# Kernel tuning notes

Measured on AMD Instinct MI355X. Metric: run time of the kernel, lower is better.

The kernel has to match this reference:

```python
import jax, jax.numpy as jnp
import numpy as np

B, T, CV, DIM = 1, 1024, 8, 2048
NH, HD, W = 32, 64, 8
BMM = NH * HD


def swa_transform(x, window):
    # x: (b, t, cv, d) -> (b, t, window*cv, d)
    # matches torch pad-front + unfold + transpose + reshape: window-major, char-minor
    b, t, cv, d = x.shape
    xp = jnp.pad(x, ((0, 0), (window - 1, 0), (0, 0), (0, 0)))
    wins = jnp.stack([xp[:, w:w + t] for w in range(window)], axis=2)  # (b,t,W,cv,d)
    return wins.reshape(b, t, window * cv, d)


def rope(x, freqs):
    # interleaved-pair RoPE (rotary_embedding_torch default, theta=10000)
    # x: (..., hd); freqs broadcastable against x[..., 0::2]
    cos, sin = jnp.cos(freqs), jnp.sin(freqs)
    x1, x2 = x[..., 0::2], x[..., 1::2]
    return jnp.stack([x1 * cos - x2 * sin, x1 * sin + x2 * cos], axis=-1).reshape(x.shape)


def setup_inputs() -> dict:
    key = jax.random.key(0)
    ks = jax.random.split(key, 6)
    s = 0.02
    return {
        "x": jax.random.normal(ks[0], (B, T, DIM), dtype=jnp.float32),
        "chars": jax.random.normal(ks[1], (B, T, CV, DIM), dtype=jnp.float32),
        "wq": jax.random.normal(ks[2], (BMM, DIM), dtype=jnp.float32) * s,
        "wk": jax.random.normal(ks[3], (BMM, DIM), dtype=jnp.float32) * s,
        "wv": jax.random.normal(ks[4], (BMM, DIM), dtype=jnp.float32) * s,
        "wo": jax.random.normal(ks[5], (DIM, BMM), dtype=jnp.float32) * s,
    }


def reference(x, chars, wq, wk, wv, wo):
    b, t = x.shape[0], x.shape[1]
    cv = chars.shape[2]
    wc = W * cv

    q = x @ wq.T                     # (b, t, BMM)
    k = chars @ wk.T                 # (b, t, cv, BMM)
    v = chars @ wv.T

    k = swa_transform(k, W)          # (b, t, W*cv, BMM)
    v = swa_transform(v, W)

    q = q.reshape(b, t, NH, HD).transpose(0, 2, 1, 3)          # (b, nh, t, hd)
    k = k.reshape(b, t, wc, NH, HD).transpose(0, 3, 1, 2, 4)   # (b, nh, t, wc, hd)
    v = v.reshape(b, t, wc, NH, HD).transpose(0, 3, 1, 2, 4)   # (b, nh, t, wc, hd)

    inv_freq = 1.0 / (10000.0 ** (jnp.arange(0, HD, 2, dtype=jnp.float32) / HD))
    freqs = jnp.arange(t, dtype=jnp.float32)[:, None] * inv_freq  # (t, hd/2)

    q = rope(q, freqs)                       # rotate over token axis (-2)
    k = rope(k, freqs[:, None, :])           # rotate over token axis (-3), broadcast over window

    scores = jnp.einsum('bhtd,bhtkd->bhtk', q, k) / np.float32(np.sqrt(HD))
    attn = jax.nn.softmax(scores, axis=-1)   # (b, nh, t, wc)
    out = jnp.einsum('bhtk,bhtkd->bhtd', attn, v)
    out = out.transpose(0, 2, 1, 3).reshape(b, t, NH * HD)
    return out @ wo.T
```

## Files before the change

### kernel.cpp

```cpp
#include <hip/hip_runtime.h>
#include <hip/hip_bf16.h>
#include <cstdint>
#include <cstddef>

static constexpr int kT   = 1024;
static constexpr int kCV  = 8;
static constexpr int kDim = 2048;
static constexpr int kNH  = 32;
static constexpr int kHD  = 64;
static constexpr int kW   = 8;
static constexpr int kK   = 2048;

using bf16_t = __hip_bfloat16;

typedef __attribute__((ext_vector_type(8))) __bf16 bf16x8;
typedef __attribute__((ext_vector_type(4))) float  f32x4;

__device__ __forceinline__ float bf_bits_to_f32(unsigned short u) {
    union { unsigned int i; float f; } c;
    c.i = ((unsigned int)u) << 16;
    return c.f;
}

struct CastArgs {
    const float* src[6];
    bf16_t*      dst[6];
    int          cum[7];
};

__global__ void cast_all(CastArgs a, int total_chunks) {
    const int c = blockIdx.x * blockDim.x + threadIdx.x;
    if (c >= total_chunks) return;
    int r = 0;
#pragma unroll
    for (int i = 1; i <= 5; ++i) r += (c >= a.cum[i]) ? 1 : 0;
    const int local = c - a.cum[r];
    const float* s = a.src[r] + (size_t)local * 8;
    bf16_t*      d = a.dst[r] + (size_t)local * 8;
    const float4 lo = *reinterpret_cast<const float4*>(s);
    const float4 hi = *reinterpret_cast<const float4*>(s + 4);
    union { bf16_t h[8]; uint4 u; } o;
    o.h[0] = __float2bfloat16(lo.x); o.h[1] = __float2bfloat16(lo.y);
    o.h[2] = __float2bfloat16(lo.z); o.h[3] = __float2bfloat16(lo.w);
    o.h[4] = __float2bfloat16(hi.x); o.h[5] = __float2bfloat16(hi.y);
    o.h[6] = __float2bfloat16(hi.z); o.h[7] = __float2bfloat16(hi.w);
    *reinterpret_cast<uint4*>(d) = o.u;
}

__device__ __forceinline__ void gemm256_body(const bf16_t* __restrict__ A,
                                             const bf16_t* __restrict__ Wt,
                                             bf16_t* __restrict__ C,
                                             int bm, int bn, int ldc,
                                             bf16_t* smem) {
    const int tid  = threadIdx.x;
    const int wave = tid >> 6;
    const int lane = tid & 63;
    const int l16  = lane & 15;
    const int quad = lane >> 4;
    const int wm   = (wave >> 2) * 128;
    const int wn   = (wave & 3) * 64;

    f32x4 acc[8][4];
#pragma unroll
    for (int i = 0; i < 8; ++i)
#pragma unroll
        for (int j = 0; j < 4; ++j) acc[i][j] = (f32x4)0.0f;

    const int srow = tid >> 3;
    const int jg   = (tid & 7) ^ (srow & 7);
    const bf16_t* gA = A  + (size_t)(bm + srow) * kK + jg * 8;
    const bf16_t* gB = Wt + (size_t)(bn + srow) * kK + jg * 8;
    const int ldsw = wave * 512;

    auto stage = [&](int kt, int p) {
        const int k0 = kt * 64;
        bf16_t* As = smem + p * 32768;
        bf16_t* Bs = As + 16384;
#pragma unroll
        for (int i = 0; i < 4; ++i)
            __builtin_amdgcn_global_load_lds(
                (const __attribute__((address_space(1))) void*)(gA + (size_t)i * 64 * kK + k0),
                (__attribute__((address_space(3))) void*)(As + i * 4096 + ldsw),
                16, 0, 0);
#pragma unroll
        for (int i = 0; i < 4; ++i)
            __builtin_amdgcn_global_load_lds(
                (const __attribute__((address_space(1))) void*)(gB + (size_t)i * 64 * kK + k0),
                (__attribute__((address_space(3))) void*)(Bs + i * 4096 + ldsw),
                16, 0, 0);
    };

    bf16x8 af[8], bq[4];
    auto rdfrags = [&](int p, int ph) {
        const bf16_t* As = smem + p * 32768;
        const bf16_t* Bs = As + 16384;
        const int jla = (ph * 4 + quad) ^ (l16 & 7);
#pragma unroll
        for (int i = 0; i < 8; ++i)
            af[i] = *reinterpret_cast<const bf16x8*>(
                &As[(wm + i * 16 + l16) * 64 + jla * 8]);
#pragma unroll
        for (int j = 0; j < 4; ++j)
            bq[j] = *reinterpret_cast<const bf16x8*>(
                &Bs[(wn + j * 16 + l16) * 64 + jla * 8]);
    };
    auto domfma = [&]() {
#pragma unroll
        for (int i = 0; i < 8; ++i)
#pragma unroll
            for (int j = 0; j < 4; ++j)
                acc[i][j] = __builtin_amdgcn_mfma_f32_16x16x32_bf16(
                    af[i], bq[j], acc[i][j], 0, 0, 0);
    };

    stage(0, 0);
    stage(1, 1);
    asm volatile("s_waitcnt vmcnt(8)" ::: "memory");
    __builtin_amdgcn_s_barrier();

    static_assert(kK / 64 == 32, "NT");
    int p = 0;
    for (int t = 0; t < 30; ++t) {
        rdfrags(p, 0);
        domfma();
        rdfrags(p, 1);
        asm volatile("s_waitcnt lgkmcnt(0)" ::: "memory");
        __builtin_amdgcn_s_barrier();
        stage(t + 2, p);
        __builtin_amdgcn_s_setprio(1);
        domfma();
        __builtin_amdgcn_s_setprio(0);
        asm volatile("s_waitcnt vmcnt(8)" ::: "memory");
        __builtin_amdgcn_s_barrier();
        p ^= 1;
    }
    rdfrags(p, 0); domfma();
    rdfrags(p, 1);
    __builtin_amdgcn_s_setprio(1);
    domfma();
    __builtin_amdgcn_s_setprio(0);
    asm volatile("s_waitcnt vmcnt(0)" ::: "memory");
    __builtin_amdgcn_s_barrier();
    p ^= 1;
    rdfrags(p, 0); domfma();
    rdfrags(p, 1); domfma();

#pragma unroll
    for (int i = 0; i < 8; ++i) {
#pragma unroll
        for (int rr = 0; rr < 4; ++rr) {
            const int row = bm + wm + i * 16 + quad * 4 + rr;
#pragma unroll
            for (int j = 0; j < 4; ++j) {
                const int col = bn + wn + j * 16 + l16;
                C[(size_t)row * ldc + col] = __float2bfloat16(acc[i][j][rr]);
            }
        }
    }
}

__global__ __launch_bounds__(512, 2) void proj256_kernel(
    const bf16_t* __restrict__ xb, const bf16_t* __restrict__ cb,
    const bf16_t* __restrict__ wqb, const bf16_t* __restrict__ wkvb,
    bf16_t* __restrict__ qb, bf16_t* __restrict__ kvb) {
    extern __shared__ bf16_t smem[];
    const int bid = blockIdx.x;
    if (bid < 512) {
        const int bm = (bid >> 4) * 256;
        const int bn = (bid & 15) * 256;
        gemm256_body(cb, wkvb, kvb, bm, bn, 4096, smem);
    } else {
        const int t  = bid - 512;
        const int bm = (t >> 3) * 256;
        const int bn = (t & 7) * 256;
        gemm256_body(xb, wqb, qb, bm, bn, 2048, smem);
    }
}

template <bool ATOMIC>
__device__ __forceinline__ void gemm_body128(const bf16_t* __restrict__ A,
                                             const bf16_t* __restrict__ Wt,
                                             float* __restrict__ C,
                                             int bm, int bn, int ldc,
                                             int kbeg, int kend) {
    __shared__ bf16_t As[128 * 64];
    __shared__ bf16_t Bs[128 * 64];

    const int tid  = threadIdx.x;
    const int wave = tid >> 6;
    const int lane = tid & 63;
    const int l16  = lane & 15;
    const int quad = lane >> 4;
    const int wm   = (wave >> 1) * 64;
    const int wn   = (wave & 1) * 64;

    f32x4 acc[4][4];
#pragma unroll
    for (int i = 0; i < 4; ++i)
#pragma unroll
        for (int j = 0; j < 4; ++j) acc[i][j] = (f32x4)0.0f;

    const int srow = tid >> 3;
    const int jgs  = (tid & 7) ^ (srow & 7);
    const bf16_t* gA = A  + (size_t)(bm + srow) * kK + jgs * 8;
    const bf16_t* gB = Wt + (size_t)(bn + srow) * kK + jgs * 8;

    for (int k0 = kbeg; k0 < kend; k0 += 64) {
#pragma unroll
        for (int i = 0; i < 4; ++i) {
            __builtin_amdgcn_global_load_lds(
                (const __attribute__((address_space(1))) void*)(gA + (size_t)i * 32 * kK + k0),
                (__attribute__((address_space(3))) void*)(As + i * 2048 + wave * 512),
                16, 0, 0);
            __builtin_amdgcn_global_load_lds(
                (const __attribute__((address_space(1))) void*)(gB + (size_t)i * 32 * kK + k0),
                (__attribute__((address_space(3))) void*)(Bs + i * 2048 + wave * 512),
                16, 0, 0);
        }
        __syncthreads();

#pragma unroll
        for (int ph = 0; ph < 2; ++ph) {
            bf16x8 af[4], bfr[4];
#pragma unroll
            for (int i = 0; i < 4; ++i) {
                const int jla = (ph * 4 + quad) ^ (l16 & 7);
                af[i]  = *reinterpret_cast<const bf16x8*>(
                    &As[(wm + i * 16 + l16) * 64 + jla * 8]);
                bfr[i] = *reinterpret_cast<const bf16x8*>(
                    &Bs[(wn + i * 16 + l16) * 64 + jla * 8]);
            }
#pragma unroll
            for (int i = 0; i < 4; ++i)
#pragma unroll
                for (int j = 0; j < 4; ++j)
                    acc[i][j] = __builtin_amdgcn_mfma_f32_16x16x32_bf16(
                        af[i], bfr[j], acc[i][j], 0, 0, 0);
        }
        __syncthreads();
    }

#pragma unroll
    for (int i = 0; i < 4; ++i) {
#pragma unroll
        for (int rr = 0; rr < 4; ++rr) {
            const int row = bm + wm + i * 16 + quad * 4 + rr;
#pragma unroll
            for (int j = 0; j < 4; ++j) {
                const int col = bn + wn + j * 16 + l16;
                if constexpr (ATOMIC) {
                    atomicAdd(&C[(size_t)row * ldc + col], acc[i][j][rr]);
                } else {
                    C[(size_t)row * ldc + col] = acc[i][j][rr];
                }
            }
        }
    }
}

__global__ __launch_bounds__(256, 3) void out_gemm(
    const bf16_t* __restrict__ ob, const bf16_t* __restrict__ wob,
    float* __restrict__ out) {
    const int tile = blockIdx.x & 127;
    const int ks   = blockIdx.x >> 7;
    const int bm = (tile >> 4) * 128;
    const int bn = (tile & 15) * 128;
    gemm_body128<true>(ob, wob, out, bm, bn, 2048, ks * 1024, ks * 1024 + 1024);
}

static constexpr int kTT   = 16;
static constexpr int kSRC  = kTT + kW - 1;
static constexpr int kROWS = kSRC * kCV;
static constexpr int kLDK  = 72;

__global__ __launch_bounds__(1024) void attn_kernel(
    const bf16_t* __restrict__ qb,
    const bf16_t* __restrict__ kvb,
    bf16_t* __restrict__ ob) {
    __shared__ unsigned short kl[kROWS * kLDK];
    __shared__ unsigned short vl[kROWS * kLDK];
    __shared__ float ql[kTT * 64];
    __shared__ float al[kTT * 64];

    const int t0   = blockIdx.x * kTT;
    const int h    = blockIdx.y;
    const int tid  = threadIdx.x;
    const int wave = tid >> 6;
    const int lane = tid & 63;

    ql[tid] = __bfloat162float(qb[(size_t)(t0 + wave) * kDim + h * kHD + lane]);

    const long long grow0 = (long long)(t0 - (kW - 1)) * kCV;
#pragma unroll
    for (int c = tid; c < kROWS * 8; c += 1024) {
        const int r   = c >> 3;
        const int sub = c & 7;
        const long long grow = grow0 + r;
        uint4 kd = make_uint4(0, 0, 0, 0), vd = make_uint4(0, 0, 0, 0);
        if (grow >= 0) {
            const size_t gb = (size_t)grow * 4096 + h * kHD + sub * 8;
            kd = *reinterpret_cast<const uint4*>(kvb + gb);
            vd = *reinterpret_cast<const uint4*>(kvb + gb + 2048);
        }
        *reinterpret_cast<uint4*>(&kl[r * kLDK + sub * 8]) = kd;
        *reinterpret_cast<uint4*>(&vl[r * kLDK + sub * 8]) = vd;
    }
    __syncthreads();

    const int r = wave * kCV + lane;
    float s = 0.0f;
#pragma unroll
    for (int c = 0; c < 8; ++c) {
        union { uint4 u; unsigned short us[8]; } kv;
        kv.u = *reinterpret_cast<const uint4*>(&kl[r * kLDK + c * 8]);
        const float4 qa = *reinterpret_cast<const float4*>(&ql[wave * 64 + c * 8]);
        const float4 qc = *reinterpret_cast<const float4*>(&ql[wave * 64 + c * 8 + 4]);
        s += bf_bits_to_f32(kv.us[0]) * qa.x + bf_bits_to_f32(kv.us[1]) * qa.y +
             bf_bits_to_f32(kv.us[2]) * qa.z + bf_bits_to_f32(kv.us[3]) * qa.w +
             bf_bits_to_f32(kv.us[4]) * qc.x + bf_bits_to_f32(kv.us[5]) * qc.y +
             bf_bits_to_f32(kv.us[6]) * qc.z + bf_bits_to_f32(kv.us[7]) * qc.w;
    }
    s *= 0.125f;

    float m = s;
#pragma unroll
    for (int off = 32; off; off >>= 1) m = fmaxf(m, __shfl_xor(m, off));
    const float e = __expf(s - m);
    float sum = e;
#pragma unroll
    for (int off = 32; off; off >>= 1) sum += __shfl_xor(sum, off);
    al[wave * 64 + lane] = e / sum;

    float o = 0.0f;
#pragma unroll
    for (int k2 = 0; k2 < 64; ++k2)
        o += al[wave * 64 + k2] * bf_bits_to_f32(vl[(wave * kCV + k2) * kLDK + lane]);
    ob[(size_t)(t0 + wave) * kDim + h * kHD + lane] = __float2bfloat16(o);
}

extern "C" void kernel_launch(void* const* d_in, const int* in_sizes, int n_in,
                              void* d_out, int out_size, void* d_ws,
                              size_t ws_size, hipStream_t stream) {
    const float* x     = (const float*)d_in[0];
    const float* chars = (const float*)d_in[1];
    const float* wq    = (const float*)d_in[2];
    const float* wk    = (const float*)d_in[3];
    const float* wv    = (const float*)d_in[4];
    const float* wo    = (const float*)d_in[5];
    float* out = (float*)d_out;

    char* p = (char*)d_ws;
    bf16_t* xb   = (bf16_t*)p; p += (size_t)kT * kDim * 2;
    bf16_t* cb   = (bf16_t*)p; p += (size_t)kT * kCV * kDim * 2;
    bf16_t* wqb  = (bf16_t*)p; p += (size_t)kDim * kDim * 2;
    bf16_t* wkvb = (bf16_t*)p; p += (size_t)2 * kDim * kDim * 2;
    bf16_t* wob  = (bf16_t*)p; p += (size_t)kDim * kDim * 2;
    bf16_t* qb   = (bf16_t*)p; p += (size_t)kT * kDim * 2;
    bf16_t* kvb  = (bf16_t*)p; p += (size_t)kT * kCV * 2 * kDim * 2;
    bf16_t* ob   = (bf16_t*)p; p += (size_t)kT * kDim * 2;

    static int attr_done = 0;
    if (!attr_done) {
        hipFuncSetAttribute(reinterpret_cast<const void*>(proj256_kernel),
                            hipFuncAttributeMaxDynamicSharedMemorySize, 131072);
        attr_done = 1;
    }

    hipMemsetAsync(out, 0, (size_t)kT * kDim * sizeof(float), stream);

    CastArgs ca;
    ca.src[0] = x;     ca.dst[0] = xb;
    ca.src[1] = chars; ca.dst[1] = cb;
    ca.src[2] = wq;    ca.dst[2] = wqb;
    ca.src[3] = wk;    ca.dst[3] = wkvb;
    ca.src[4] = wv;    ca.dst[4] = wkvb + (size_t)kDim * kDim;
    ca.src[5] = wo;    ca.dst[5] = wob;
    const int sizes[6] = {kT * kDim, kT * kCV * kDim, kDim * kDim,
                          kDim * kDim, kDim * kDim, kDim * kDim};
    int cum = 0;
    ca.cum[0] = 0;
    for (int i = 0; i < 6; ++i) { cum += sizes[i] / 8; ca.cum[i + 1] = cum; }
    cast_all<<<dim3((cum + 255) / 256), dim3(256), 0, stream>>>(ca, cum);

    proj256_kernel<<<dim3(544), dim3(512), 131072, stream>>>(
        xb, cb, wqb, wkvb, qb, kvb);

    attn_kernel<<<dim3(kT / kTT, kNH), dim3(1024), 0, stream>>>(qb, kvb, ob);

    out_gemm<<<dim3(256), dim3(256), 0, stream>>>(ob, wob, out);
}
```

Baseline: 386.8 us.

## Rework projection GEMM into 8-phase pipeline and split Q GEMM into 128 tiles

The 256x256 KV projection GEMM now runs an 8-phase schedule. Each phase loads a 32-row slice of A fragments and issues one half-tile global-to-LDS stage, so memory traffic is spread across the MFMA work instead of arriving in bursts. The Q projection switches from 32 blocks of 256x256 to 128 blocks of 128x128 using a simpler single-buffered kernel, which raises the block count for the tail. The change adds many more barriers per k-step, and the simpler Q path drops double buffering. The unused non-atomic template path in the output GEMM is removed.

```diff
diff --git a/kernel.cpp b/kernel.cpp
--- a/kernel.cpp
+++ b/kernel.cpp
@@ -47,18 +47,21 @@
     *reinterpret_cast<uint4*>(d) = o.u;
 }
 
-__device__ __forceinline__ void gemm256_body(const bf16_t* __restrict__ A,
-                                             const bf16_t* __restrict__ Wt,
-                                             bf16_t* __restrict__ C,
-                                             int bm, int bn, int ldc,
-                                             bf16_t* smem) {
+__device__ __forceinline__ void gemm256_8ph(const bf16_t* __restrict__ A,
+                                            const bf16_t* __restrict__ Wt,
+                                            bf16_t* __restrict__ C,
+                                            int bm, int bn, int ldc,
+                                            bf16_t* smem) {
     const int tid  = threadIdx.x;
     const int wave = tid >> 6;
     const int lane = tid & 63;
     const int l16  = lane & 15;
     const int quad = lane >> 4;
-    const int wm   = (wave >> 2) * 128;
-    const int wn   = (wave & 3) * 64;
+    const int wmi  = wave >> 2;
+    const int wni  = wave & 3;
+
+    const int slot0 = quad ^ (l16 & 7);
+    const int slot1 = slot0 ^ 4;
 
     f32x4 acc[8][4];
 #pragma unroll
@@ -67,99 +70,201 @@
         for (int j = 0; j < 4; ++j) acc[i][j] = (f32x4)0.0f;
 
     const int srow = tid >> 3;
-    const int jg   = (tid & 7) ^ (srow & 7);
-    const bf16_t* gA = A  + (size_t)(bm + srow) * kK + jg * 8;
-    const bf16_t* gB = Wt + (size_t)(bn + srow) * kK + jg * 8;
+    const int jg8  = (((tid & 7) ^ (srow & 7))) * 8;
+    const bf16_t* gAlo = A  + (size_t)(bm + srow) * kK + jg8;
+    const bf16_t* gAhi = gAlo + (size_t)128 * kK;
+    const bf16_t* gBlo = Wt + (size_t)(bn + srow) * kK + jg8;
+    const bf16_t* gBhi = gBlo + (size_t)128 * kK;
     const int ldsw = wave * 512;
 
-    auto stage = [&](int kt, int p) {
-        const int k0 = kt * 64;
-        bf16_t* As = smem + p * 32768;
-        bf16_t* Bs = As + 16384;
-#pragma unroll
-        for (int i = 0; i < 4; ++i)
+    auto stageA = [&](int tau, int hs) {
+        bf16_t* dst = smem + (tau & 1) * 32768 + hs * 8192 + ldsw;
+        const bf16_t* src = (hs ? gAhi : gAlo) + tau * 64;
+        __builtin_amdgcn_global_load_lds(
+            (const __attribute__((address_space(1))) void*)src,
+            (__attribute__((address_space(3))) void*)dst, 16, 0, 0);
+        __builtin_amdgcn_global_load_lds(
+            (const __attribute__((address_space(1))) void*)(src + (size_t)64 * kK),
+            (__attribute__((address_space(3))) void*)(dst + 4096), 16, 0, 0);
+    };
+    auto stageB = [&](int tau, int hs) {
+        bf16_t* dst = smem + (tau & 1) * 32768 + 16384 + hs * 8192 + ldsw;
+        const bf16_t* src = (hs ? gBhi : gBlo) + tau * 64;
+        __builtin_amdgcn_global_load_lds(
+            (const __attribute__((address_space(1))) void*)src,
+            (__attribute__((address_space(3))) void*)dst, 16, 0, 0);
+        __builtin_amdgcn_global_load_lds(
+            (const __attribute__((address_space(1))) void*)(src + (size_t)64 * kK),
+            (__attribute__((address_space(3))) void*)(dst + 4096), 16, 0, 0);
+    };
+
+    bf16x8 bq0[4], bq1[4];
+
+#define PH(P, Q, STG, VMW)                                                     \
+    {                                                                          \
+        const bf16_t* Ab = smem + (P) * 32768;                                 \
+        const bf16_t* Bb = Ab + 16384;                                         \
+        bf16x8 a0[2], a1[2];                                                   \
+        _Pragma("unroll")                                                      \
+        for (int ii = 0; ii < 2; ++ii) {                                       \
+            const int rb = (wmi * 128 + ((Q) * 2 + ii) * 16 + l16) * 64;       \
+            a0[ii] = *reinterpret_cast<const bf16x8*>(&Ab[rb + slot0 * 8]);    \
+            a1[ii] = *reinterpret_cast<const bf16x8*>(&Ab[rb + slot1 * 8]);    \
+        }                                                                      \
+        if ((Q) == 0) {                                                        \
+            _Pragma("unroll")                                                  \
+            for (int j = 0; j < 4; ++j) {                                      \
+                const int rb = (wni * 64 + j * 16 + l16) * 64;                 \
+                bq0[j] = *reinterpret_cast<const bf16x8*>(&Bb[rb + slot0 * 8]);\
+                bq1[j] = *reinterpret_cast<const bf16x8*>(&Bb[rb + slot1 * 8]);\
+            }                                                                  \
+        }                                                                      \
+        STG;                                                                   \
+        __builtin_amdgcn_s_barrier();                                          \
+        asm volatile("s_waitcnt lgkmcnt(0)" ::: "memory");                     \
+        __builtin_amdgcn_s_setprio(1);                                         \
+        _Pragma("unroll")                                                      \
+        for (int ii = 0; ii < 2; ++ii)                                         \
+            _Pragma("unroll")                                                  \
+            for (int j = 0; j < 4; ++j)                                        \
+                acc[(Q) * 2 + ii][j] = __builtin_amdgcn_mfma_f32_16x16x32_bf16(\
+                    a0[ii], bq0[j], acc[(Q) * 2 + ii][j], 0, 0, 0);            \
+        _Pragma("unroll")                                                      \
+        for (int ii = 0; ii < 2; ++ii)                                         \
+            _Pragma("unroll")                                                  \
+            for (int j = 0; j < 4; ++j)                                        \
+                acc[(Q) * 2 + ii][j] = __builtin_amdgcn_mfma_f32_16x16x32_bf16(\
+                    a1[ii], bq1[j], acc[(Q) * 2 + ii][j], 0, 0, 0);            \
+        __builtin_amdgcn_s_setprio(0);                                         \
+        VMW;                                                                   \
+        __builtin_amdgcn_s_barrier();                                          \
+    }
+
+#define VM4 asm volatile("s_waitcnt vmcnt(4)" ::: "memory")
+#define VM0 asm volatile("s_waitcnt vmcnt(0)" ::: "memory")
+
+    stageB(0, 1); stageB(0, 0); stageA(0, 1); stageA(0, 0);
+    stageB(1, 1); stageB(1, 0);
+    VM4;
+    __builtin_amdgcn_s_barrier();
+
+    for (int tt = 0; tt < 15; ++tt) {
+        const int t = tt * 2;
+        PH(0, 0, stageA(t + 1, 1), (void)0)
+        PH(0, 1, stageA(t + 1, 0), (void)0)
+        PH(0, 2, stageB(t + 2, 1), (void)0)
+        PH(0, 3, stageB(t + 2, 0), VM4)
+        PH(1, 0, stageA(t + 2, 1), (void)0)
+        PH(1, 1, stageA(t + 2, 0), (void)0)
+        PH(1, 2, stageB(t + 3, 1), (void)0)
+        PH(1, 3, stageB(t + 3, 0), VM4)
+    }
+    PH(0, 0, stageA(31, 1), (void)0)
+    PH(0, 1, stageA(31, 0), (void)0)
+    PH(0, 2, (void)0, (void)0)
+    PH(0, 3, (void)0, VM0)
+    PH(1, 0, (void)0, (void)0)
+    PH(1, 1, (void)0, (void)0)
+    PH(1, 2, (void)0, (void)0)
+    PH(1, 3, (void)0, (void)0)
+
+#undef PH
+#undef VM4
+#undef VM0
+
+#pragma unroll
+    for (int i = 0; i < 8; ++i) {
+#pragma unroll
+        for (int rr = 0; rr < 4; ++rr) {
+            const int row = bm + wmi * 128 + i * 16 + quad * 4 + rr;
+#pragma unroll
+            for (int j = 0; j < 4; ++j) {
+                const int col = bn + wni * 64 + j * 16 + l16;
+                C[(size_t)row * ldc + col] = __float2bfloat16(acc[i][j][rr]);
+            }
+        }
+    }
+}
+
+__device__ __forceinline__ void gemm128_8w(const bf16_t* __restrict__ A,
+                                           const bf16_t* __restrict__ Wt,
+                                           bf16_t* __restrict__ C,
+                                           int bm, int bn, int ldc,
+                                           bf16_t* smem) {
+    const int tid  = threadIdx.x;
+    const int wave = tid >> 6;
+    const int lane = tid & 63;
+    const int l16  = lane & 15;
+    const int quad = lane >> 4;
+    const int wmi  = wave >> 2;
+    const int wni  = wave & 3;
+
+    bf16_t* As = smem;
+    bf16_t* Bs = smem + 8192;
+
+    f32x4 acc[4][2];
+#pragma unroll
+    for (int i = 0; i < 4; ++i)
+#pragma unroll
+        for (int j = 0; j < 2; ++j) acc[i][j] = (f32x4)0.0f;
+
+    const int srow = tid >> 3;
+    const int jg8  = (((tid & 7) ^ (srow & 7))) * 8;
+    const bf16_t* gA = A  + (size_t)(bm + srow) * kK + jg8;
+    const bf16_t* gB = Wt + (size_t)(bn + srow) * kK + jg8;
+    const int ldsw = wave * 512;
+
+    for (int k0 = 0; k0 < kK; k0 += 64) {
+#pragma unroll
+        for (int i = 0; i < 2; ++i) {
             __builtin_amdgcn_global_load_lds(
                 (const __attribute__((address_space(1))) void*)(gA + (size_t)i * 64 * kK + k0),
                 (__attribute__((address_space(3))) void*)(As + i * 4096 + ldsw),
                 16, 0, 0);
-#pragma unroll
-        for (int i = 0; i < 4; ++i)
             __builtin_amdgcn_global_load_lds(
                 (const __attribute__((address_space(1))) void*)(gB + (size_t)i * 64 * kK + k0),
                 (__attribute__((address_space(3))) void*)(Bs + i * 4096 + ldsw),
                 16, 0, 0);
-    };
-
-    bf16x8 af[8], bq[4];
-    auto rdfrags = [&](int p, int ph) {
-        const bf16_t* As = smem + p * 32768;
-        const bf16_t* Bs = As + 16384;
-        const int jla = (ph * 4 + quad) ^ (l16 & 7);
-#pragma unroll
-        for (int i = 0; i < 8; ++i)
-            af[i] = *reinterpret_cast<const bf16x8*>(
-                &As[(wm + i * 16 + l16) * 64 + jla * 8]);
-#pragma unroll
-        for (int j = 0; j < 4; ++j)
-            bq[j] = *reinterpret_cast<const bf16x8*>(
-                &Bs[(wn + j * 16 + l16) * 64 + jla * 8]);
-    };
-    auto domfma = [&]() {
-#pragma unroll
-        for (int i = 0; i < 8; ++i)
-#pragma unroll
-            for (int j = 0; j < 4; ++j)
-                acc[i][j] = __builtin_amdgcn_mfma_f32_16x16x32_bf16(
-                    af[i], bq[j], acc[i][j], 0, 0, 0);
-    };
-
-    stage(0, 0);
-    stage(1, 1);
-    asm volatile("s_waitcnt vmcnt(8)" ::: "memory");
-    __builtin_amdgcn_s_barrier();
-
-    static_assert(kK / 64 == 32, "NT");
-    int p = 0;
-    for (int t = 0; t < 30; ++t) {
-        rdfrags(p, 0);
-        domfma();
-        rdfrags(p, 1);
-        asm volatile("s_waitcnt lgkmcnt(0)" ::: "memory");
-        __builtin_amdgcn_s_barrier();
-        stage(t + 2, p);
-        __builtin_amdgcn_s_setprio(1);
-        domfma();
-        __builtin_amdgcn_s_setprio(0);
-        asm volatile("s_waitcnt vmcnt(8)" ::: "memory");
-        __builtin_amdgcn_s_barrier();
-        p ^= 1;
-    }
-    rdfrags(p, 0); domfma();
-    rdfrags(p, 1);
-    __builtin_amdgcn_s_setprio(1);
-    domfma();
-    __builtin_amdgcn_s_setprio(0);
-    asm volatile("s_waitcnt vmcnt(0)" ::: "memory");
-    __builtin_amdgcn_s_barrier();
-    p ^= 1;
-    rdfrags(p, 0); domfma();
-    rdfrags(p, 1); domfma();
-
-#pragma unroll
-    for (int i = 0; i < 8; ++i) {
+        }
+        __syncthreads();
+
+#pragma unroll
+        for (int ph = 0; ph < 2; ++ph) {
+            const int jla = (ph * 4 + quad) ^ (l16 & 7);
+            bf16x8 af[4], bfr[2];
+#pragma unroll
+            for (int i = 0; i < 4; ++i)
+                af[i] = *reinterpret_cast<const bf16x8*>(
+                    &As[(wmi * 64 + i * 16 + l16) * 64 + jla * 8]);
+#pragma unroll
+            for (int j = 0; j < 2; ++j)
+                bfr[j] = *reinterpret_cast<const bf16x8*>(
+                    &Bs[(wni * 32 + j * 16 + l16) * 64 + jla * 8]);
+#pragma unroll
+            for (int i = 0; i < 4; ++i)
+#pragma unroll
+                for (int j = 0; j < 2; ++j)
+                    acc[i][j] = __builtin_amdgcn_mfma_f32_16x16x32_bf16(
+                        af[i], bfr[j], acc[i][j], 0, 0, 0);
+        }
+        __syncthreads();
+    }
+
+#pragma unroll
+    for (int i = 0; i < 4; ++i) {
 #pragma unroll
         for (int rr = 0; rr < 4; ++rr) {
-            const int row = bm + wm + i * 16 + quad * 4 + rr;
-#pragma unroll
-            for (int j = 0; j < 4; ++j) {
-                const int col = bn + wn + j * 16 + l16;
+            const int row = bm + wmi * 64 + i * 16 + quad * 4 + rr;
+#pragma unroll
+            for (int j = 0; j < 2; ++j) {
+                const int col = bn + wni * 32 + j * 16 + l16;
                 C[(size_t)row * ldc + col] = __float2bfloat16(acc[i][j][rr]);
             }
         }
     }
 }
 
-__global__ __launch_bounds__(512, 2) void proj256_kernel(
+__global__ __launch_bounds__(512, 2) void proj8_kernel(
     const bf16_t* __restrict__ xb, const bf16_t* __restrict__ cb,
     const bf16_t* __restrict__ wqb, const bf16_t* __restrict__ wkvb,
     bf16_t* __restrict__ qb, bf16_t* __restrict__ kvb) {
@@ -168,16 +273,15 @@
     if (bid < 512) {
         const int bm = (bid >> 4) * 256;
         const int bn = (bid & 15) * 256;
-        gemm256_body(cb, wkvb, kvb, bm, bn, 4096, smem);
+        gemm256_8ph(cb, wkvb, kvb, bm, bn, 4096, smem);
     } else {
         const int t  = bid - 512;
-        const int bm = (t >> 3) * 256;
-        const int bn = (t & 7) * 256;
-        gemm256_body(xb, wqb, qb, bm, bn, 2048, smem);
-    }
-}
-
-template <bool ATOMIC>
+        const int bm = (t >> 4) * 128;
+        const int bn = (t & 15) * 128;
+        gemm128_8w(xb, wqb, qb, bm, bn, 2048, smem);
+    }
+}
+
 __device__ __forceinline__ void gemm_body128(const bf16_t* __restrict__ A,
                                              const bf16_t* __restrict__ Wt,
                                              float* __restrict__ C,
@@ -248,11 +352,7 @@
 #pragma unroll
             for (int j = 0; j < 4; ++j) {
                 const int col = bn + wn + j * 16 + l16;
-                if constexpr (ATOMIC) {
-                    atomicAdd(&C[(size_t)row * ldc + col], acc[i][j][rr]);
-                } else {
-                    C[(size_t)row * ldc + col] = acc[i][j][rr];
-                }
+                atomicAdd(&C[(size_t)row * ldc + col], acc[i][j][rr]);
             }
         }
     }
@@ -265,7 +365,7 @@
     const int ks   = blockIdx.x >> 7;
     const int bm = (tile >> 4) * 128;
     const int bn = (tile & 15) * 128;
-    gemm_body128<true>(ob, wob, out, bm, bn, 2048, ks * 1024, ks * 1024 + 1024);
+    gemm_body128(ob, wob, out, bm, bn, 2048, ks * 1024, ks * 1024 + 1024);
 }
 
 static constexpr int kTT   = 16;
@@ -361,7 +461,7 @@
 
     static int attr_done = 0;
     if (!attr_done) {
-        hipFuncSetAttribute(reinterpret_cast<const void*>(proj256_kernel),
+        hipFuncSetAttribute(reinterpret_cast<const void*>(proj8_kernel),
                             hipFuncAttributeMaxDynamicSharedMemorySize, 131072);
         attr_done = 1;
     }
@@ -382,7 +482,7 @@
     for (int i = 0; i < 6; ++i) { cum += sizes[i] / 8; ca.cum[i + 1] = cum; }
     cast_all<<<dim3((cum + 255) / 256), dim3(256), 0, stream>>>(ca, cum);
 
-    proj256_kernel<<<dim3(544), dim3(512), 131072, stream>>>(
+    proj8_kernel<<<dim3(640), dim3(512), 131072, stream>>>(
         xb, cb, wqb, wkvb, qb, kvb);
 
     attn_kernel<<<dim3(kT / kTT, kNH), dim3(1024), 0, stream>>>(qb, kvb, ob);
```

After: 371.6 us. -3.9%, faster.
